# Performance work log

Hardware: AMD Instinct MI355X
Metric: run time of the kernel (lower is better)

## Reference

```python
import jax, jax.numpy as jnp
import numpy as np
from jax import lax

CLIP = 10.0


def setup_inputs() -> dict:
    key = jax.random.key(0)
    k1, k2, k3, k4 = jax.random.split(key, 4)
    B, T, I, H = 64, 512, 512, 512
    x = jax.random.normal(k1, (B, T, I), dtype=jnp.float32)
    kernel = jax.random.normal(k2, (I, H), dtype=jnp.float32) * 0.05
    recurrent_kernel = jax.random.normal(k3, (H, H), dtype=jnp.float32) * 0.05
    bias_i = jax.random.normal(k4, (H,), dtype=jnp.float32) * 0.05
    h0 = jnp.zeros((B, H), dtype=jnp.float32)
    return {"x": x, "kernel": kernel, "recurrent_kernel": recurrent_kernel,
            "bias_i": bias_i, "h0": h0}


def reference(x, kernel, recurrent_kernel, bias_i, h0):
    # Elman RNN: Ht = tanh(clip(Xt@W + Ht-1@R + b, -clip, clip))
    def step(h, xt):
        g = xt @ kernel + h @ recurrent_kernel + bias_i  # [B, H]
        h_new = jnp.tanh(jnp.clip(g, -CLIP, CLIP))
        return h_new, h_new

    xs = jnp.swapaxes(x, 0, 1)  # [T, B, I] for scan over time
    h_last, ys = lax.scan(step, h0, xs)
    outputs = jnp.swapaxes(ys, 0, 1)  # [B, T, H]
    return outputs, h_last
```

## Files before the change

kernel.cpp:

```cpp
#include <hip/hip_runtime.h>

#define Bdim 64
#define Tdim 512
#define Idim 512
#define Hdim 512
#define CLIPV 10.0f
#define NREGP 48
#define NLDSP 16

typedef __attribute__((ext_vector_type(4))) float f32x4;
typedef __attribute__((ext_vector_type(8))) short bf16x8;
typedef _Float16 half2v __attribute__((ext_vector_type(2)));

__device__ __forceinline__ ushort f2bf(float f) {
    unsigned u = __builtin_bit_cast(unsigned, f);
    u += 0x7fffu + ((u >> 16) & 1u);
    return (ushort)(u >> 16);
}
__device__ __forceinline__ float bf2f(ushort h) {
    return __builtin_bit_cast(float, (unsigned)h << 16);
}
__device__ __forceinline__ void split_bf(float f, ushort& h, ushort& l) {
    h = f2bf(f);
    l = f2bf(f - bf2f(h));
}
__device__ __forceinline__ float dot2acc(uint r, uint h2, float acc) {
#if __has_builtin(__builtin_amdgcn_fdot2)
    return __builtin_amdgcn_fdot2(__builtin_bit_cast(half2v, r),
                                  __builtin_bit_cast(half2v, h2), acc, false);
#else
    half2v a = __builtin_bit_cast(half2v, r);
    half2v b = __builtin_bit_cast(half2v, h2);
    return acc + (float)a.x * (float)b.x + (float)a.y * (float)b.y;
#endif
}
__device__ __forceinline__ uint vcomp(uint4 v, int i) {
    return i == 0 ? v.x : i == 1 ? v.y : i == 2 ? v.z : v.w;
}
__device__ __forceinline__ uint packf16(float a, float b) {
    _Float16 fa = (_Float16)a, fb = (_Float16)b;
    return (uint)__builtin_bit_cast(ushort, fa) |
           ((uint)__builtin_bit_cast(ushort, fb) << 16);
}

__global__ __launch_bounds__(256) void transpose_w_kernel(const float* __restrict__ w,
                                                          ushort* __restrict__ wth,
                                                          ushort* __restrict__ wtl) {
    int idx = blockIdx.x * 256 + threadIdx.x;
    int k = idx >> 9, n = idx & 511;
    ushort h, l;
    split_bf(w[idx], h, l);
    wth[n * Idim + k] = h;
    wtl[n * Idim + k] = l;
}

__global__ __launch_bounds__(256) void pack_r_kernel(const float* __restrict__ Rw,
                                                     uint* __restrict__ rpk) {
    int d = blockIdx.x * 256 + threadIdx.x;
    int i = d >> 11;
    int rem = d & 2047;
    int t = rem >> 2, q = rem & 3;
    int k = (t >> 7) * 128 + 2 * i;
    int c = ((t & 127) << 2) + q;
    rpk[d] = packf16(Rw[(size_t)k * Hdim + c], Rw[(size_t)(k + 1) * Hdim + c]);
}

#define BM 128
#define BN 128
#define BK 32
__global__ __launch_bounds__(256) void gemm_xw(
    const float* __restrict__ A,
    const ushort* __restrict__ Bth,
    const ushort* __restrict__ Btl,
    const float* __restrict__ bias,
    float* __restrict__ C,
    int M, int N, int K)
{
    __shared__ ushort AsH[BM][BK];
    __shared__ ushort AsL[BM][BK];
    __shared__ ushort BsH[BN][BK];
    __shared__ ushort BsL[BN][BK];
    int bm = blockIdx.x, bn = blockIdx.y;
    int tid = threadIdx.x;
    int wave = tid >> 6, lane = tid & 63;
    int wr = wave >> 1, wc = wave & 1;
    f32x4 acc[4][4] = {};
    const int row0 = bm * BM, col0 = bn * BN;
    const int sr = tid >> 1;
    const int sc = (tid & 1) * 16;

    for (int kt = 0; kt < K; kt += BK) {
        const float* gA = A + (size_t)(row0 + sr) * K + kt + sc;
        #pragma unroll
        for (int q = 0; q < 4; ++q) {
            float4 v = *(const float4*)(gA + q * 4);
            ushort4 h4, l4;
            split_bf(v.x, h4.x, l4.x);
            split_bf(v.y, h4.y, l4.y);
            split_bf(v.z, h4.z, l4.z);
            split_bf(v.w, h4.w, l4.w);
            *(ushort4*)&AsH[sr][sc + q * 4] = h4;
            *(ushort4*)&AsL[sr][sc + q * 4] = l4;
        }
        const int4* gBh = (const int4*)(Bth + (size_t)(col0 + sr) * K + kt + sc);
        *(int4*)&BsH[sr][sc]     = gBh[0];
        *(int4*)&BsH[sr][sc + 8] = gBh[1];
        const int4* gBl = (const int4*)(Btl + (size_t)(col0 + sr) * K + kt + sc);
        *(int4*)&BsL[sr][sc]     = gBl[0];
        *(int4*)&BsL[sr][sc + 8] = gBl[1];
        __syncthreads();

        const int r = lane & 15, kg = lane >> 4;
        bf16x8 ah[4], al[4], bh[4], bl[4];
        #pragma unroll
        for (int m = 0; m < 4; ++m) {
            ah[m] = *(const bf16x8*)&AsH[wr * 64 + m * 16 + r][kg * 8];
            al[m] = *(const bf16x8*)&AsL[wr * 64 + m * 16 + r][kg * 8];
        }
        #pragma unroll
        for (int n = 0; n < 4; ++n) {
            bh[n] = *(const bf16x8*)&BsH[wc * 64 + n * 16 + r][kg * 8];
            bl[n] = *(const bf16x8*)&BsL[wc * 64 + n * 16 + r][kg * 8];
        }
        #pragma unroll
        for (int m = 0; m < 4; ++m)
            #pragma unroll
            for (int n = 0; n < 4; ++n) {
                acc[m][n] = __builtin_amdgcn_mfma_f32_16x16x32_bf16(ah[m], bh[n], acc[m][n], 0, 0, 0);
                acc[m][n] = __builtin_amdgcn_mfma_f32_16x16x32_bf16(ah[m], bl[n], acc[m][n], 0, 0, 0);
                acc[m][n] = __builtin_amdgcn_mfma_f32_16x16x32_bf16(al[m], bh[n], acc[m][n], 0, 0, 0);
            }
        __syncthreads();
    }

    const int cl = lane & 15, rg = lane >> 4;
    #pragma unroll
    for (int n = 0; n < 4; ++n) {
        int gc = col0 + wc * 64 + n * 16 + cl;
        float bv = bias[gc];
        #pragma unroll
        for (int m = 0; m < 4; ++m) {
            int gr = row0 + wr * 64 + m * 16 + rg * 4;
            #pragma unroll
            for (int r2 = 0; r2 < 4; ++r2)
                C[(size_t)(gr + r2) * N + gc] = acc[m][n][r2] + bv;
        }
    }
}

__global__ __launch_bounds__(512, 2) void rnn_reg_kernel(
    const uint* __restrict__ Rpk,
    float* __restrict__ out,
    float* __restrict__ hlast,
    const float* __restrict__ h0)
{
    __shared__ uint Rlds[NLDSP * 2048];
    __shared__ uint h2[Hdim / 2];
    __shared__ float part[4][Hdim];

    const int tid = threadIdx.x;
    const int row = blockIdx.x;
    const int kq  = tid >> 7;
    const int c0  = (tid & 127) * 4;
    const int hb  = kq * 64;

    uint4 rr4[NREGP];
    const uint* rbase = Rpk + tid * 4;
    #pragma unroll
    for (int i = 0; i < NREGP; ++i)
        rr4[i] = *(const uint4*)(rbase + i * 2048);
    #pragma unroll
    for (int ip = 0; ip < NLDSP; ++ip)
        *(uint4*)&Rlds[ip * 2048 + tid * 4] =
            *(const uint4*)(rbase + (NREGP + ip) * 2048);

    if (tid < 256)
        h2[tid] = packf16(h0[row * Hdim + 2 * tid], h0[row * Hdim + 2 * tid + 1]);
    __syncthreads();

    float* orow = out + (size_t)row * Tdim * Hdim;

    for (int t = 0; t < Tdim; ++t, orow += Hdim) {
        f32x4 pre = {};
        if (tid < 128) pre = *(const f32x4*)(orow + c0);

        float a0 = 0.f, a1 = 0.f, a2 = 0.f, a3 = 0.f;
        #pragma unroll
        for (int ch = 0; ch < 12; ++ch) {
            uint4 hh = *(const uint4*)&h2[hb + ch * 4];
            #pragma unroll
            for (int i = 0; i < 4; ++i) {
                uint hv = vcomp(hh, i);
                uint4 rv = rr4[ch * 4 + i];
                a0 = dot2acc(rv.x, hv, a0);
                a1 = dot2acc(rv.y, hv, a1);
                a2 = dot2acc(rv.z, hv, a2);
                a3 = dot2acc(rv.w, hv, a3);
            }
        }
        #pragma unroll
        for (int ch = 0; ch < 4; ++ch) {
            uint4 hh = *(const uint4*)&h2[hb + 48 + ch * 4];
            #pragma unroll
            for (int i = 0; i < 4; ++i) {
                uint hv = vcomp(hh, i);
                uint4 rv = *(const uint4*)&Rlds[(ch * 4 + i) * 2048 + tid * 4];
                a0 = dot2acc(rv.x, hv, a0);
                a1 = dot2acc(rv.y, hv, a1);
                a2 = dot2acc(rv.z, hv, a2);
                a3 = dot2acc(rv.w, hv, a3);
            }
        }
        part[kq][c0 + 0] = a0;
        part[kq][c0 + 1] = a1;
        part[kq][c0 + 2] = a2;
        part[kq][c0 + 3] = a3;
        __syncthreads();

        if (tid < 128) {
            f32x4 p0 = *(const f32x4*)&part[0][c0];
            f32x4 p1 = *(const f32x4*)&part[1][c0];
            f32x4 p2 = *(const f32x4*)&part[2][c0];
            f32x4 p3 = *(const f32x4*)&part[3][c0];
            float g0 = p0[0] + p1[0] + p2[0] + p3[0] + pre[0];
            float g1 = p0[1] + p1[1] + p2[1] + p3[1] + pre[1];
            float g2 = p0[2] + p1[2] + p2[2] + p3[2] + pre[2];
            float g3 = p0[3] + p1[3] + p2[3] + p3[3] + pre[3];
            g0 = fminf(fmaxf(g0, -CLIPV), CLIPV);
            g1 = fminf(fmaxf(g1, -CLIPV), CLIPV);
            g2 = fminf(fmaxf(g2, -CLIPV), CLIPV);
            g3 = fminf(fmaxf(g3, -CLIPV), CLIPV);
            float v0 = tanhf(g0), v1 = tanhf(g1), v2 = tanhf(g2), v3 = tanhf(g3);
            f32x4 hv = {v0, v1, v2, v3};
            *(f32x4*)(orow + c0) = hv;
            h2[(c0 >> 1) + 0] = packf16(v0, v1);
            h2[(c0 >> 1) + 1] = packf16(v2, v3);
            if (t == Tdim - 1)
                *(f32x4*)&hlast[row * Hdim + c0] = hv;
        }
        __syncthreads();
    }
}

extern "C" void kernel_launch(void* const* d_in, const int* in_sizes, int n_in,
                              void* d_out, int out_size, void* d_ws, size_t ws_size,
                              hipStream_t stream) {
    const float* x    = (const float*)d_in[0];
    const float* W    = (const float*)d_in[1];
    const float* R    = (const float*)d_in[2];
    const float* bias = (const float*)d_in[3];
    const float* h0   = (const float*)d_in[4];
    float* out = (float*)d_out;

    ushort* wth = (ushort*)d_ws;
    ushort* wtl = wth + (size_t)Idim * Hdim;
    uint* rpk   = (uint*)((char*)d_ws + (1u << 20));

    transpose_w_kernel<<<(Idim * Hdim + 255) / 256, 256, 0, stream>>>(W, wth, wtl);
    pack_r_kernel<<<512, 256, 0, stream>>>(R, rpk);

    dim3 gg(Bdim * Tdim / BM, Hdim / BN);
    gemm_xw<<<gg, 256, 0, stream>>>(x, wth, wtl, bias, out, Bdim * Tdim, Hdim, Idim);

    rnn_reg_kernel<<<Bdim, 512, 0, stream>>>(
        rpk, out, out + (size_t)Bdim * Tdim * Hdim, h0);
}
```

Before: 960.9 us.

## Broadcast h via readlane, spread epilogue over all threads, use fast tanh

Replaces per-thread LDS reads of the hidden state with one LDS load per lane followed by readlane broadcasts. The reduce/tanh epilogue now runs on all 512 threads with one element each, where before 128 threads handled four each. tanhf is replaced with an exp/reciprocal formula. The register/LDS split of R moves from 48/16 to 52/12. Together these aim to shorten the serial per-timestep critical path, at the cost of more register pressure and slightly lower tanh accuracy.

```diff
diff --git a/kernel.cpp b/kernel.cpp
--- a/kernel.cpp
+++ b/kernel.cpp
@@ -5,8 +5,8 @@
 #define Idim 512
 #define Hdim 512
 #define CLIPV 10.0f
-#define NREGP 48
-#define NLDSP 16
+#define NREGP 52
+#define NLDSP 12
 
 typedef __attribute__((ext_vector_type(4))) float f32x4;
 typedef __attribute__((ext_vector_type(8))) short bf16x8;
@@ -34,13 +34,21 @@
     return acc + (float)a.x * (float)b.x + (float)a.y * (float)b.y;
 #endif
 }
-__device__ __forceinline__ uint vcomp(uint4 v, int i) {
-    return i == 0 ? v.x : i == 1 ? v.y : i == 2 ? v.z : v.w;
-}
 __device__ __forceinline__ uint packf16(float a, float b) {
     _Float16 fa = (_Float16)a, fb = (_Float16)b;
     return (uint)__builtin_bit_cast(ushort, fa) |
            ((uint)__builtin_bit_cast(ushort, fb) << 16);
+}
+__device__ __forceinline__ ushort f2h(float f) {
+    _Float16 h = (_Float16)f;
+    return __builtin_bit_cast(ushort, h);
+}
+__device__ __forceinline__ float fastrcp(float x) {
+#if __has_builtin(__builtin_amdgcn_rcpf)
+    return __builtin_amdgcn_rcpf(x);
+#else
+    return 1.0f / x;
+#endif
 }
 
 __global__ __launch_bounds__(256) void transpose_w_kernel(const float* __restrict__ w,
@@ -155,14 +163,15 @@
     const float* __restrict__ h0)
 {
     __shared__ uint Rlds[NLDSP * 2048];
-    __shared__ uint h2[Hdim / 2];
+    __shared__ ushort h1[Hdim];
     __shared__ float part[4][Hdim];
 
-    const int tid = threadIdx.x;
-    const int row = blockIdx.x;
-    const int kq  = tid >> 7;
-    const int c0  = (tid & 127) * 4;
-    const int hb  = kq * 64;
+    const int tid  = threadIdx.x;
+    const int row  = blockIdx.x;
+    const int kq   = tid >> 7;
+    const int lane = tid & 63;
+    const int c0   = (tid & 127) * 4;
+    const int hb   = kq * 64;
 
     uint4 rr4[NREGP];
     const uint* rbase = Rpk + tid * 4;
@@ -174,70 +183,44 @@
         *(uint4*)&Rlds[ip * 2048 + tid * 4] =
             *(const uint4*)(rbase + (NREGP + ip) * 2048);
 
-    if (tid < 256)
-        h2[tid] = packf16(h0[row * Hdim + 2 * tid], h0[row * Hdim + 2 * tid + 1]);
+    h1[tid] = f2h(h0[row * Hdim + tid]);
     __syncthreads();
 
     float* orow = out + (size_t)row * Tdim * Hdim;
 
     for (int t = 0; t < Tdim; ++t, orow += Hdim) {
-        f32x4 pre = {};
-        if (tid < 128) pre = *(const f32x4*)(orow + c0);
+        float pre = orow[tid];
+        uint hval = ((const uint*)h1)[hb + lane];
 
         float a0 = 0.f, a1 = 0.f, a2 = 0.f, a3 = 0.f;
         #pragma unroll
-        for (int ch = 0; ch < 12; ++ch) {
-            uint4 hh = *(const uint4*)&h2[hb + ch * 4];
-            #pragma unroll
-            for (int i = 0; i < 4; ++i) {
-                uint hv = vcomp(hh, i);
-                uint4 rv = rr4[ch * 4 + i];
-                a0 = dot2acc(rv.x, hv, a0);
-                a1 = dot2acc(rv.y, hv, a1);
-                a2 = dot2acc(rv.z, hv, a2);
-                a3 = dot2acc(rv.w, hv, a3);
-            }
-        }
-        #pragma unroll
-        for (int ch = 0; ch < 4; ++ch) {
-            uint4 hh = *(const uint4*)&h2[hb + 48 + ch * 4];
-            #pragma unroll
-            for (int i = 0; i < 4; ++i) {
-                uint hv = vcomp(hh, i);
-                uint4 rv = *(const uint4*)&Rlds[(ch * 4 + i) * 2048 + tid * 4];
-                a0 = dot2acc(rv.x, hv, a0);
-                a1 = dot2acc(rv.y, hv, a1);
-                a2 = dot2acc(rv.z, hv, a2);
-                a3 = dot2acc(rv.w, hv, a3);
-            }
-        }
-        part[kq][c0 + 0] = a0;
-        part[kq][c0 + 1] = a1;
-        part[kq][c0 + 2] = a2;
-        part[kq][c0 + 3] = a3;
-        __syncthreads();
-
-        if (tid < 128) {
-            f32x4 p0 = *(const f32x4*)&part[0][c0];
-            f32x4 p1 = *(const f32x4*)&part[1][c0];
-            f32x4 p2 = *(const f32x4*)&part[2][c0];
-            f32x4 p3 = *(const f32x4*)&part[3][c0];
-            float g0 = p0[0] + p1[0] + p2[0] + p3[0] + pre[0];
-            float g1 = p0[1] + p1[1] + p2[1] + p3[1] + pre[1];
-            float g2 = p0[2] + p1[2] + p2[2] + p3[2] + pre[2];
-            float g3 = p0[3] + p1[3] + p2[3] + p3[3] + pre[3];
-            g0 = fminf(fmaxf(g0, -CLIPV), CLIPV);
-            g1 = fminf(fmaxf(g1, -CLIPV), CLIPV);
-            g2 = fminf(fmaxf(g2, -CLIPV), CLIPV);
-            g3 = fminf(fmaxf(g3, -CLIPV), CLIPV);
-            float v0 = tanhf(g0), v1 = tanhf(g1), v2 = tanhf(g2), v3 = tanhf(g3);
-            f32x4 hv = {v0, v1, v2, v3};
-            *(f32x4*)(orow + c0) = hv;
-            h2[(c0 >> 1) + 0] = packf16(v0, v1);
-            h2[(c0 >> 1) + 1] = packf16(v2, v3);
-            if (t == Tdim - 1)
-                *(f32x4*)&hlast[row * Hdim + c0] = hv;
-        }
+        for (int i = 0; i < NREGP; ++i) {
+            uint hvi = __builtin_amdgcn_readlane(hval, i);
+            uint4 rv = rr4[i];
+            a0 = dot2acc(rv.x, hvi, a0);
+            a1 = dot2acc(rv.y, hvi, a1);
+            a2 = dot2acc(rv.z, hvi, a2);
+            a3 = dot2acc(rv.w, hvi, a3);
+        }
+        #pragma unroll
+        for (int i = 0; i < NLDSP; ++i) {
+            uint hvi = __builtin_amdgcn_readlane(hval, NREGP + i);
+            uint4 rv = *(const uint4*)&Rlds[i * 2048 + tid * 4];
+            a0 = dot2acc(rv.x, hvi, a0);
+            a1 = dot2acc(rv.y, hvi, a1);
+            a2 = dot2acc(rv.z, hvi, a2);
+            a3 = dot2acc(rv.w, hvi, a3);
+        }
+        *(f32x4*)&part[kq][c0] = (f32x4){a0, a1, a2, a3};
+        __syncthreads();
+
+        float s = part[0][tid] + part[1][tid] + part[2][tid] + part[3][tid] + pre;
+        s = fminf(fmaxf(s, -CLIPV), CLIPV);
+        float e = __expf(2.0f * s);
+        float v = (e - 1.0f) * fastrcp(e + 1.0f);
+        orow[tid] = v;
+        h1[tid] = f2h(v);
+        if (t == Tdim - 1) hlast[row * Hdim + tid] = v;
         __syncthreads();
     }
 }
```

Result: faster. 815.3 us (-15.2%).
